# Performance work log

Hardware: AMD Instinct MI355X
Metric: run time of the kernel (lower is better)

Reference implementation:

```python
import jax, jax.numpy as jnp
import numpy as np

D_MODEL = 256; N_LAYERS = 4; INPUT_LEN = 15
D_INNER = 512; D_STATE = 16; D_CONV = 4; DT_RANK = 16
BATCH = 4; SEQ = 2048; EPS = 1e-5

def _ln(x, w, b):
    m = jnp.mean(x, -1, keepdims=True)
    v = jnp.var(x, -1, keepdims=True)
    return (x - m) * jax.lax.rsqrt(v + EPS) * w + b

def _silu(x):
    return x * jax.nn.sigmoid(x)

def _mixer(h, inW, cw, cb, xpW, dtW, dtb, A_log, Dp, opW):
    # h: [B,L,d_model]
    xz = h @ inW.T                      # [B,L,2*D_INNER]
    xh, z = jnp.split(xz, 2, axis=-1)
    # causal depthwise conv1d
    xc = jnp.transpose(xh, (0, 2, 1))   # [B,D,L]
    xc = jax.lax.conv_general_dilated(xc, cw, (1,), [(D_CONV - 1, 0)],
                                      feature_group_count=D_INNER,
                                      dimension_numbers=('NCH', 'OIH', 'NCH'))
    xc = xc + cb[None, :, None]
    xh = _silu(jnp.transpose(xc, (0, 2, 1)))  # [B,L,D]
    dbl = xh @ xpW.T                    # [B,L,DT_RANK+2N]
    dt = dbl[..., :DT_RANK]
    Bm = dbl[..., DT_RANK:DT_RANK + D_STATE]
    C = dbl[..., DT_RANK + D_STATE:]
    dt = jax.nn.softplus(dt @ dtW.T + dtb)    # [B,L,D]
    A = -jnp.exp(A_log)                       # [D,N]
    dA = jnp.exp(dt[..., None] * A)           # [B,L,D,N]
    dBu = dt[..., None] * Bm[:, :, None, :] * xh[..., None]  # [B,L,D,N]
    def step(hst, inp):
        dA_t, dBu_t, C_t = inp
        hst = dA_t * hst + dBu_t
        y = jnp.einsum('bdn,bn->bd', hst, C_t)
        return hst, y
    h0 = jnp.zeros((xh.shape[0], D_INNER, D_STATE), xh.dtype)
    _, ys = jax.lax.scan(step, h0, (jnp.transpose(dA, (1, 0, 2, 3)),
                                    jnp.transpose(dBu, (1, 0, 2, 3)),
                                    jnp.transpose(C, (1, 0, 2))))
    y = jnp.transpose(ys, (1, 0, 2)) + Dp * xh
    y = y * _silu(z)
    return y @ opW.T

def setup_inputs():
    key = jax.random.key(0)
    ks = jax.random.split(key, 8)
    s = 0.02
    return {
        'x_src': jax.random.normal(ks[0], (BATCH, SEQ, INPUT_LEN), jnp.float32),
        'single_eval_pos': 1024,
        'in_W': jax.random.normal(ks[1], (D_MODEL, INPUT_LEN)) * s,
        'norm_w': jnp.ones((N_LAYERS, D_MODEL)),
        'norm_b': jnp.zeros((N_LAYERS, D_MODEL)),
        'inproj_W': jax.random.normal(ks[2], (N_LAYERS, 2 * D_INNER, D_MODEL)) * s,
        'conv_w': jax.random.normal(ks[3], (N_LAYERS, D_INNER, 1, D_CONV)) * 0.2,
        'conv_b': jnp.zeros((N_LAYERS, D_INNER)),
        'xproj_W': jax.random.normal(ks[4], (N_LAYERS, DT_RANK + 2 * D_STATE, D_INNER)) * s,
        'dtproj_W': jax.random.normal(ks[5], (N_LAYERS, D_INNER, DT_RANK)) * 0.1,
        'dtproj_b': jnp.log(jnp.expm1(jnp.full((N_LAYERS, D_INNER), 0.01))),
        'A_log': jnp.log(jnp.broadcast_to(jnp.arange(1, D_STATE + 1, dtype=jnp.float32), (N_LAYERS, D_INNER, D_STATE)) + 0.0),
        'D_param': jnp.ones((N_LAYERS, D_INNER)),
        'outproj_W': jax.random.normal(ks[6], (N_LAYERS, D_MODEL, D_INNER)) * s,
        'out_W': jax.random.normal(ks[7], (1, D_MODEL)) * s,
    }

def reference(x_src, single_eval_pos, in_W, norm_w, norm_b, inproj_W, conv_w, conv_b, xproj_W, dtproj_W, dtproj_b, A_log, D_param, outproj_W, out_W):
    h = x_src @ in_W.T                  # [B,L,d_model]
    res = None
    for i in range(N_LAYERS):
        res = h if res is None else h + res
        hn = _ln(res, norm_w[i], norm_b[i])
        h = _mixer(hn, inproj_W[i], conv_w[i], conv_b[i], xproj_W[i],
                   dtproj_W[i], dtproj_b[i], A_log[i], D_param[i], outproj_W[i])
    # backbone returns hidden_states directly (norm_f defined but not applied)
    return h @ out_W.T                  # [B,L,1]
```

## Files before the change

kernel.cpp:

```cpp
#include <hip/hip_runtime.h>

#define B_   4
#define T_   2048
#define BT_  8192
#define INL  15
#define DM   256
#define DI   512
#define DX   1024
#define DS_  16
#define DR_  16
#define NO_  48
#define NL   4
#define NC_  128
#define LCH  16

#define N0C  (NL*DX*DM/4)
#define N1C  (NL*DM*DI/4)
#define N2C  (NL*NO_*DI/4)
#define NCVT ((N0C + N1C + N2C + DI + 255)/256)
#define NINL (BT_/4)

typedef short bf16x8 __attribute__((ext_vector_type(8)));
typedef float f32x4  __attribute__((ext_vector_type(4)));

__device__ __forceinline__ float sigmoidf_(float x){
    return __builtin_amdgcn_rcpf(1.f + __expf(-x));
}
__device__ __forceinline__ float softplusf_(float x){
    return fmaxf(x, 0.f) + __logf(1.f + __expf(-fabsf(x)));
}

__device__ __forceinline__ unsigned short f2bf(float x){
    union { float f; unsigned u; } v; v.f = x;
    unsigned r = (v.u + 0x7FFFu + ((v.u >> 16) & 1u)) >> 16;
    return (unsigned short)r;
}
__device__ __forceinline__ float bf2f(unsigned short h){
    union { unsigned u; float f; } v; v.u = ((unsigned)h) << 16;
    return v.f;
}

__device__ __forceinline__ void ld16(const float* __restrict__ p, float* v){
    const float4* q = (const float4*)p;
    float4 x0=q[0],x1=q[1],x2=q[2],x3=q[3];
    v[0]=x0.x; v[1]=x0.y; v[2]=x0.z; v[3]=x0.w;
    v[4]=x1.x; v[5]=x1.y; v[6]=x1.z; v[7]=x1.w;
    v[8]=x2.x; v[9]=x2.y; v[10]=x2.z; v[11]=x2.w;
    v[12]=x3.x; v[13]=x3.y; v[14]=x3.z; v[15]=x3.w;
}
__device__ __forceinline__ void st16(float* __restrict__ p, const float* v){
    float4* q = (float4*)p;
    q[0] = make_float4(v[0],v[1],v[2],v[3]);
    q[1] = make_float4(v[4],v[5],v[6],v[7]);
    q[2] = make_float4(v[8],v[9],v[10],v[11]);
    q[3] = make_float4(v[12],v[13],v[14],v[15]);
}

__global__ void k_init(const float* __restrict__ W0, unsigned short* __restrict__ h0,
                       unsigned short* __restrict__ l0,
                       const float* __restrict__ W1, unsigned short* __restrict__ h1,
                       unsigned short* __restrict__ l1,
                       const float* __restrict__ W2, unsigned short* __restrict__ h2,
                       unsigned short* __restrict__ l2,
                       const float* __restrict__ opW3, const float* __restrict__ outW,
                       float* __restrict__ cwc,
                       const float* __restrict__ x, const float* __restrict__ W,
                       float* __restrict__ res,
                       unsigned short* __restrict__ hnhi, unsigned short* __restrict__ hnlo,
                       const float* __restrict__ w, const float* __restrict__ b){
    int bid = blockIdx.x;
    if(bid < NCVT){
        int g = bid*256 + threadIdx.x;
        const float* Wp; unsigned short *hi, *lo; int idx;
        if(g < N0C){ Wp = W0; hi = h0; lo = l0; idx = g; }
        else if(g < N0C+N1C){ Wp = W1; hi = h1; lo = l1; idx = g - N0C; }
        else if(g < N0C+N1C+N2C){ Wp = W2; hi = h2; lo = l2; idx = g - N0C - N1C; }
        else {
            int k = g - (N0C+N1C+N2C);
            if(k < DI){
                float s = 0.f;
#pragma unroll 8
                for(int m=0;m<DM;m++) s += outW[m]*opW3[(size_t)m*DI + k];
                cwc[k] = s;
            }
            return;
        }
        float4 v = ((const float4*)Wp)[idx];
        ushort4 h, l;
        h.x = f2bf(v.x); l.x = f2bf(v.x - bf2f(h.x));
        h.y = f2bf(v.y); l.y = f2bf(v.y - bf2f(h.y));
        h.z = f2bf(v.z); l.z = f2bf(v.z - bf2f(h.z));
        h.w = f2bf(v.w); l.w = f2bf(v.w - bf2f(h.w));
        ((ushort4*)hi)[idx] = h;
        ((ushort4*)lo)[idx] = l;
        return;
    }
    int wv = threadIdx.x >> 6, lane = threadIdx.x & 63;
    int bt = (bid - NCVT)*4 + wv;
    const float* xr = x + bt*INL;
    float xl[INL];
#pragma unroll
    for(int k=0;k<INL;k++) xl[k] = xr[k];
    float4 v;
    float* vv = (float*)&v;
#pragma unroll
    for(int j=0;j<4;j++){
        int m = lane*4 + j;
        const float* wr = W + m*INL;
        float acc = 0.f;
#pragma unroll
        for(int k=0;k<INL;k++) acc += xl[k]*wr[k];
        vv[j] = acc;
    }
    ((float4*)(res + (size_t)bt*DM))[lane] = v;
    float s  = v.x+v.y+v.z+v.w;
    float ss = v.x*v.x+v.y*v.y+v.z*v.z+v.w*v.w;
#pragma unroll
    for(int m=1;m<64;m<<=1){ s += __shfl_xor(s,m); ss += __shfl_xor(ss,m); }
    float mean = s*(1.f/DM);
    float var  = ss*(1.f/DM) - mean*mean;
    float inv  = rsqrtf(var + 1e-5f);
    float4 wt = ((const float4*)w)[lane];
    float4 bs = ((const float4*)b)[lane];
    float4 o;
    o.x = (v.x-mean)*inv*wt.x + bs.x;
    o.y = (v.y-mean)*inv*wt.y + bs.y;
    o.z = (v.z-mean)*inv*wt.z + bs.z;
    o.w = (v.w-mean)*inv*wt.w + bs.w;
    ushort4 hh, ll;
    hh.x = f2bf(o.x); ll.x = f2bf(o.x - bf2f(hh.x));
    hh.y = f2bf(o.y); ll.y = f2bf(o.y - bf2f(hh.y));
    hh.z = f2bf(o.z); ll.z = f2bf(o.z - bf2f(hh.z));
    hh.w = f2bf(o.w); ll.w = f2bf(o.w - bf2f(hh.w));
    ((ushort4*)(hnhi + (size_t)bt*DM))[lane] = hh;
    ((ushort4*)(hnlo + (size_t)bt*DM))[lane] = ll;
}

__global__ void k_resln(const float* __restrict__ res,
                        unsigned short* __restrict__ hnhi, unsigned short* __restrict__ hnlo,
                        const float* __restrict__ w, const float* __restrict__ b){
    int wv = threadIdx.x >> 6, lane = threadIdx.x & 63;
    int bt = blockIdx.x*4 + wv;
    float4 v = ((const float4*)(res + (size_t)bt*DM))[lane];
    float s  = v.x+v.y+v.z+v.w;
    float ss = v.x*v.x+v.y*v.y+v.z*v.z+v.w*v.w;
#pragma unroll
    for(int m=1;m<64;m<<=1){ s += __shfl_xor(s,m); ss += __shfl_xor(ss,m); }
    float mean = s*(1.f/DM);
    float var  = ss*(1.f/DM) - mean*mean;
    float inv  = rsqrtf(var + 1e-5f);
    float4 wt = ((const float4*)w)[lane];
    float4 bs = ((const float4*)b)[lane];
    float4 o;
    o.x = (v.x-mean)*inv*wt.x + bs.x;
    o.y = (v.y-mean)*inv*wt.y + bs.y;
    o.z = (v.z-mean)*inv*wt.z + bs.z;
    o.w = (v.w-mean)*inv*wt.w + bs.w;
    ushort4 hh, ll;
    hh.x = f2bf(o.x); ll.x = f2bf(o.x - bf2f(hh.x));
    hh.y = f2bf(o.y); ll.y = f2bf(o.y - bf2f(hh.y));
    hh.z = f2bf(o.z); ll.z = f2bf(o.z - bf2f(hh.z));
    hh.w = f2bf(o.w); ll.w = f2bf(o.w - bf2f(hh.w));
    ((ushort4*)(hnhi + (size_t)bt*DM))[lane] = hh;
    ((ushort4*)(hnlo + (size_t)bt*DM))[lane] = ll;
}

template<int BM,int BN>
__global__ void __launch_bounds__(256) k_gemm_bf3(
    const unsigned short* __restrict__ Ahi, const unsigned short* __restrict__ Alo,
    const unsigned short* __restrict__ Bhi, const unsigned short* __restrict__ Blo,
    float* __restrict__ C, int M, int N, int K)
{
    constexpr int LDP = 40;
    constexpr int WM = BM/2, WN = BN/2;
    constexpr int MI_ = WM/16, NI_ = WN/16;
    __shared__ unsigned short sAh[BM*LDP], sAl[BM*LDP], sBh[BN*LDP], sBl[BN*LDP];
    int tid  = threadIdx.x;
    int wave = tid >> 6, lane = tid & 63;
    int wm0  = (wave >> 1) * WM, wn0 = (wave & 1) * WN;
    int m0   = blockIdx.y * BM, n0 = blockIdx.x * BN;
    int lr   = lane & 15;
    int kq   = (lane >> 4) * 8;
    int quad4 = (lane >> 4) * 4;

    f32x4 acc[MI_][NI_];
#pragma unroll
    for(int i=0;i<MI_;i++)
#pragma unroll
        for(int j=0;j<NI_;j++) acc[i][j] = (f32x4){0.f,0.f,0.f,0.f};

    for(int k0=0;k0<K;k0+=32){
#pragma unroll
        for(int i=tid;i<BM*4;i+=256){
            int r = i>>2, cg2 = (i&3)*8;
            size_t go = (size_t)(m0+r)*K + k0 + cg2;
            *(float4*)(&sAh[r*LDP + cg2]) = *(const float4*)(Ahi + go);
            *(float4*)(&sAl[r*LDP + cg2]) = *(const float4*)(Alo + go);
        }
#pragma unroll
        for(int i=tid;i<BN*4;i+=256){
            int r = i>>2, cg2 = (i&3)*8;
            size_t go = (size_t)(n0+r)*K + k0 + cg2;
            *(float4*)(&sBh[r*LDP + cg2]) = *(const float4*)(Bhi + go);
            *(float4*)(&sBl[r*LDP + cg2]) = *(const float4*)(Blo + go);
        }
        __syncthreads();
        bf16x8 ah[MI_], al[MI_], bh[NI_], bl[NI_];
#pragma unroll
        for(int mi=0;mi<MI_;mi++){
            int ro = (wm0 + mi*16 + lr)*LDP + kq;
            ah[mi] = *(const bf16x8*)(&sAh[ro]);
            al[mi] = *(const bf16x8*)(&sAl[ro]);
        }
#pragma unroll
        for(int ni=0;ni<NI_;ni++){
            int ro = (wn0 + ni*16 + lr)*LDP + kq;
            bh[ni] = *(const bf16x8*)(&sBh[ro]);
            bl[ni] = *(const bf16x8*)(&sBl[ro]);
        }
#pragma unroll
        for(int mi=0;mi<MI_;mi++)
#pragma unroll
            for(int ni=0;ni<NI_;ni++){
                acc[mi][ni] = __builtin_amdgcn_mfma_f32_16x16x32_bf16(ah[mi], bh[ni], acc[mi][ni], 0,0,0);
                acc[mi][ni] = __builtin_amdgcn_mfma_f32_16x16x32_bf16(ah[mi], bl[ni], acc[mi][ni], 0,0,0);
                acc[mi][ni] = __builtin_amdgcn_mfma_f32_16x16x32_bf16(al[mi], bh[ni], acc[mi][ni], 0,0,0);
            }
        __syncthreads();
    }
#pragma unroll
    for(int mi=0;mi<MI_;mi++)
#pragma unroll
        for(int ni=0;ni<NI_;ni++){
            int col = n0 + wn0 + ni*16 + lr;
#pragma unroll
            for(int r=0;r<4;r++){
                int row = m0 + wm0 + mi*16 + quad4 + r;
                C[(size_t)row*N + col] = acc[mi][ni][r];
            }
        }
}

__global__ void __launch_bounds__(256) k_gemm_pk_res(
    const unsigned* __restrict__ Apk,
    const unsigned short* __restrict__ Bhi, const unsigned short* __restrict__ Blo,
    float* __restrict__ res)
{
    constexpr int BM = 64, BN = 64, K = 512, LDP = 40;
    __shared__ unsigned short sAh[BM*LDP], sAl[BM*LDP], sBh[BN*LDP], sBl[BN*LDP];
    int tid  = threadIdx.x;
    int wave = tid >> 6, lane = tid & 63;
    int wm0  = (wave >> 1) * 32, wn0 = (wave & 1) * 32;
    int m0   = blockIdx.y * BM, n0 = blockIdx.x * BN;
    int lr   = lane & 15;
    int kq   = (lane >> 4) * 8;
    int quad4 = (lane >> 4) * 4;

    f32x4 acc[2][2];
#pragma unroll
    for(int i=0;i<2;i++)
#pragma unroll
        for(int j=0;j<2;j++) acc[i][j] = (f32x4){0.f,0.f,0.f,0.f};

    for(int k0=0;k0<K;k0+=32){
        if(tid < BM*2){
            int r = tid>>1, hf = (tid&1)*16;
            const uint4* yp = (const uint4*)(Apk + (size_t)(m0+r)*K + k0 + hf);
#pragma unroll
            for(int q=0;q<4;q++){
                uint4 p = yp[q];
                ushort4 H, L;
                H.x=(unsigned short)p.x;  L.x=(unsigned short)(p.x>>16);
                H.y=(unsigned short)p.y;  L.y=(unsigned short)(p.y>>16);
                H.z=(unsigned short)p.z;  L.z=(unsigned short)(p.z>>16);
                H.w=(unsigned short)p.w;  L.w=(unsigned short)(p.w>>16);
                *(ushort4*)(&sAh[r*LDP + hf + q*4]) = H;
                *(ushort4*)(&sAl[r*LDP + hf + q*4]) = L;
            }
        }
        {
            int r = tid>>2, cg2 = (tid&3)*8;
            size_t go = (size_t)(n0+r)*K + k0 + cg2;
            *(float4*)(&sBh[r*LDP + cg2]) = *(const float4*)(Bhi + go);
            *(float4*)(&sBl[r*LDP + cg2]) = *(const float4*)(Blo + go);
        }
        __syncthreads();
        bf16x8 ah[2], al[2], bh[2], bl[2];
#pragma unroll
        for(int mi=0;mi<2;mi++){
            int ro = (wm0 + mi*16 + lr)*LDP + kq;
            ah[mi] = *(const bf16x8*)(&sAh[ro]);
            al[mi] = *(const bf16x8*)(&sAl[ro]);
        }
#pragma unroll
        for(int ni=0;ni<2;ni++){
            int ro = (wn0 + ni*16 + lr)*LDP + kq;
            bh[ni] = *(const bf16x8*)(&sBh[ro]);
            bl[ni] = *(const bf16x8*)(&sBl[ro]);
        }
#pragma unroll
        for(int mi=0;mi<2;mi++)
#pragma unroll
            for(int ni=0;ni<2;ni++){
                acc[mi][ni] = __builtin_amdgcn_mfma_f32_16x16x32_bf16(ah[mi], bh[ni], acc[mi][ni], 0,0,0);
                acc[mi][ni] = __builtin_amdgcn_mfma_f32_16x16x32_bf16(ah[mi], bl[ni], acc[mi][ni], 0,0,0);
                acc[mi][ni] = __builtin_amdgcn_mfma_f32_16x16x32_bf16(al[mi], bh[ni], acc[mi][ni], 0,0,0);
            }
        __syncthreads();
    }
#pragma unroll
    for(int mi=0;mi<2;mi++)
#pragma unroll
        for(int ni=0;ni<2;ni++){
            int col = n0 + wn0 + ni*16 + lr;
#pragma unroll
            for(int r=0;r<4;r++){
                int row = m0 + wm0 + mi*16 + quad4 + r;
                size_t o = (size_t)row*DM + col;
                res[o] += acc[mi][ni][r];
            }
        }
}

__global__ void __launch_bounds__(512) k_convxp2(
    const float* __restrict__ xz, const float* __restrict__ cw, const float* __restrict__ cb,
    const unsigned short* __restrict__ Bhi, const unsigned short* __restrict__ Blo,
    const float* __restrict__ dtW, const float* __restrict__ dtbias,
    const float* __restrict__ A_log,
    float* __restrict__ dbl,
    float* __restrict__ S, float* __restrict__ sdt)
{
    __shared__ unsigned short sAh[16*520], sAl[16*520];
    __shared__ float sP[6][16][20];
    __shared__ float sD[16*52];

    int tid = threadIdx.x;
    int wave = tid >> 6, lane = tid & 63;
    int lr = lane & 15, kq = (lane>>4)*8, quad4 = (lane>>4)*4;
    int m0 = blockIdx.x * LCH;
    int d  = tid;
    int nt = wave >> 1, kh = wave & 1;

    float xv[19];
    {
        int rbase = m0 - 3;
        bool mask0 = ((m0 & (T_-1)) == 0);
#pragma unroll
        for(int j=0;j<19;j++)
            xv[j] = (mask0 && j<3) ? 0.f : xz[(size_t)(rbase+j)*DX + d];
    }
    float4 w4 = *(const float4*)(cw + d*4);
    float bias = cb[d];
    float vh[16];
#pragma unroll
    for(int t=0;t<16;t++){
        float a = bias + w4.x*xv[t] + w4.y*xv[t+1] + w4.z*xv[t+2] + w4.w*xv[t+3];
        float v = a * sigmoidf_(a);
        vh[t] = v;
        unsigned short hh = f2bf(v);
        sAh[t*520 + d] = hh;
        sAl[t*520 + d] = f2bf(v - bf2f(hh));
    }
    __syncthreads();

    if(wave < 6){
        const unsigned short* bhp = Bhi + (size_t)(nt*16 + lr)*DI + kh*256 + kq;
        const unsigned short* blp = Blo + (size_t)(nt*16 + lr)*DI + kh*256 + kq;
        f32x4 acc = {0.f,0.f,0.f,0.f};
#pragma unroll 4
        for(int ks=0;ks<8;ks++){
            int ao = lr*520 + kh*256 + ks*32 + kq;
            bf16x8 ah = *(const bf16x8*)(&sAh[ao]);
            bf16x8 al = *(const bf16x8*)(&sAl[ao]);
            bf16x8 bh = *(const bf16x8*)(bhp + ks*32);
            bf16x8 bl = *(const bf16x8*)(blp + ks*32);
            acc = __builtin_amdgcn_mfma_f32_16x16x32_bf16(ah, bh, acc, 0,0,0);
            acc = __builtin_amdgcn_mfma_f32_16x16x32_bf16(ah, bl, acc, 0,0,0);
            acc = __builtin_amdgcn_mfma_f32_16x16x32_bf16(al, bh, acc, 0,0,0);
        }
#pragma unroll
        for(int r=0;r<4;r++) sP[wave][quad4+r][lr] = acc[r];
    }
    __syncthreads();

    for(int i=tid;i<768;i+=512){
        int t = i/48, n = i - t*48;
        int nt2 = n >> 4, nn = n & 15;
        float v = sP[nt2*2][t][nn] + sP[nt2*2+1][t][nn];
        dbl[(size_t)(m0+t)*48 + n] = v;
        sD[t*52 + n] = v;
    }
    __syncthreads();

    float a_[16]; ld16(A_log + (size_t)d*16, a_);
#pragma unroll
    for(int n=0;n<16;n++) a_[n] = -__expf(a_[n]);
    float wr_[16]; ld16(dtW + (size_t)d*16, wr_);
    float bsv = dtbias[d];
    int b = m0 >> 11;
    int c = (m0 & (T_-1)) >> 4;
    float st_[16];
#pragma unroll
    for(int n=0;n<16;n++) st_[n] = 0.f;
    float sd = 0.f;
#pragma unroll 4
    for(int t=0;t<16;t++){
        float dl[16]; ld16(&sD[t*52], dl);
        float bv[16]; ld16(&sD[t*52 + 16], bv);
        float pre = bsv;
#pragma unroll
        for(int r=0;r<16;r++) pre += dl[r]*wr_[r];
        float dtv = softplusf_(pre);
        float dx = dtv*vh[t];
        sd += dtv;
#pragma unroll
        for(int n=0;n<16;n++) st_[n] = __expf(dtv*a_[n])*st_[n] + dx*bv[n];
    }
    st16(S + (((size_t)b*NC_ + c)*DI + d)*16, st_);
    sdt[((size_t)b*NC_ + c)*DI + d] = sd;
}

__global__ void k_scan2(const float* __restrict__ S, const float* __restrict__ sdt,
                        const float* __restrict__ A_log, float* __restrict__ Hinit){
    int g = blockIdx.x*128 + threadIdx.x;
    int b = g >> 13;
    int dn = g & 8191;
    int d = dn >> 4;
    float a = -__expf(A_log[dn]);
    float H = 0.f;
    for(int c0=0;c0<NC_;c0+=8){
        float sv[8], gv[8];
#pragma unroll
        for(int j=0;j<8;j++){
            sv[j] = S[((size_t)(b*NC_ + c0 + j))*8192 + dn];
            gv[j] = sdt[(size_t)(b*NC_ + c0 + j)*DI + d];
        }
#pragma unroll
        for(int j=0;j<8;j++){
            size_t o = ((size_t)(b*NC_ + c0 + j))*8192 + dn;
            Hinit[o] = H;
            H = __expf(gv[j]*a)*H + sv[j];
        }
    }
}

__global__ void __launch_bounds__(256) k_scan3(
    const float* __restrict__ dbl, const float* __restrict__ xz,
    const float* __restrict__ cvw, const float* __restrict__ cvb,
    const float* __restrict__ A_log, const float* __restrict__ Dpar,
    const float* __restrict__ dtW, const float* __restrict__ dtbias,
    const float* __restrict__ Hinit, unsigned* __restrict__ Y)
{
    __shared__ float sbc[16*52];
    int tid = threadIdx.x;
    int c = blockIdx.y, b = blockIdx.z;
    int m0 = b*T_ + c*LCH;
    if(tid < 192){
        int t = tid/12, s = tid - t*12;
        *(float4*)(&sbc[t*52 + s*4]) = *(const float4*)(dbl + (size_t)(m0+t)*48 + s*4);
    }
    __syncthreads();
    int d = blockIdx.x*256 + tid;
    float xv[19];
    {
        int rbase = m0 - 3;
        bool mask0 = (c == 0);
#pragma unroll
        for(int j=0;j<19;j++)
            xv[j] = (mask0 && j<3) ? 0.f : xz[(size_t)(rbase+j)*DX + d];
    }
    float zvp[16];
#pragma unroll
    for(int t=0;t<16;t++) zvp[t] = xz[(size_t)(m0+t)*DX + DI + d];
    float4 w4 = *(const float4*)(cvw + d*4);
    float bias = cvb[d];
    float xhp[16];
#pragma unroll
    for(int t=0;t<16;t++){
        float a = bias + w4.x*xv[t] + w4.y*xv[t+1] + w4.z*xv[t+2] + w4.w*xv[t+3];
        xhp[t] = a * sigmoidf_(a);
    }
    float a_[16]; ld16(A_log + (size_t)d*16, a_);
#pragma unroll
    for(int n=0;n<16;n++) a_[n] = -__expf(a_[n]);
    float wr_[16]; ld16(dtW + (size_t)d*16, wr_);
    float bsv = dtbias[d];
    float st_[16]; ld16(Hinit + (((size_t)b*NC_ + c)*DI + d)*16, st_);
    float Dp = Dpar[d];
#pragma unroll 2
    for(int t=0;t<LCH;t++){
        int bt = m0 + t;
        float dl[16]; ld16(&sbc[t*52], dl);
        float bv[16]; ld16(&sbc[t*52 + 16], bv);
        float cv[16]; ld16(&sbc[t*52 + 32], cv);
        float pre = bsv;
#pragma unroll
        for(int r=0;r<16;r++) pre += dl[r]*wr_[r];
        float dtv = softplusf_(pre);
        float xhv = xhp[t];
        float dx = dtv*xhv;
        float y = 0.f;
#pragma unroll
        for(int n=0;n<16;n++){
            st_[n] = __expf(dtv*a_[n])*st_[n] + dx*bv[n];
            y += st_[n]*cv[n];
        }
        float zv = zvp[t];
        y += Dp*xhv;
        y = y * zv * sigmoidf_(zv);
        unsigned short hh = f2bf(y);
        unsigned short ll = f2bf(y - bf2f(hh));
        Y[(size_t)bt*DI + d] = (unsigned)hh | ((unsigned)ll << 16);
    }
}

__global__ void __launch_bounds__(512) k_scan3o(
    const float* __restrict__ dbl, const float* __restrict__ xz,
    const float* __restrict__ cvw, const float* __restrict__ cvb,
    const float* __restrict__ A_log, const float* __restrict__ Dpar,
    const float* __restrict__ dtW, const float* __restrict__ dtbias,
    const float* __restrict__ Hinit, const float* __restrict__ cwc,
    float* __restrict__ out)
{
    __shared__ float sbc[16*52];
    __shared__ float sW[8][16];
    int tid = threadIdx.x;
    int c = blockIdx.x, b = blockIdx.y;
    int m0 = b*T_ + c*LCH;
    if(tid < 192){
        int t = tid/12, s = tid - t*12;
        *(float4*)(&sbc[t*52 + s*4]) = *(const float4*)(dbl + (size_t)(m0+t)*48 + s*4);
    }
    __syncthreads();
    int d = tid;
    int wave = tid >> 6, lane = tid & 63;
    float xv[19];
    {
        int rbase = m0 - 3;
        bool mask0 = (c == 0);
#pragma unroll
        for(int j=0;j<19;j++)
            xv[j] = (mask0 && j<3) ? 0.f : xz[(size_t)(rbase+j)*DX + d];
    }
    float zvp[16];
#pragma unroll
    for(int t=0;t<16;t++) zvp[t] = xz[(size_t)(m0+t)*DX + DI + d];
    float4 w4 = *(const float4*)(cvw + d*4);
    float bias = cvb[d];
    float xhp[16];
#pragma unroll
    for(int t=0;t<16;t++){
        float a = bias + w4.x*xv[t] + w4.y*xv[t+1] + w4.z*xv[t+2] + w4.w*xv[t+3];
        xhp[t] = a * sigmoidf_(a);
    }
    float a_[16]; ld16(A_log + (size_t)d*16, a_);
#pragma unroll
    for(int n=0;n<16;n++) a_[n] = -__expf(a_[n]);
    float wr_[16]; ld16(dtW + (size_t)d*16, wr_);
    float bsv = dtbias[d];
    float st_[16]; ld16(Hinit + (((size_t)b*NC_ + c)*DI + d)*16, st_);
    float Dp = Dpar[d];
    float cwv = cwc[d];
#pragma unroll 2
    for(int t=0;t<LCH;t++){
        float dl[16]; ld16(&sbc[t*52], dl);
        float bv[16]; ld16(&sbc[t*52 + 16], bv);
        float cv[16]; ld16(&sbc[t*52 + 32], cv);
        float pre = bsv;
#pragma unroll
        for(int r=0;r<16;r++) pre += dl[r]*wr_[r];
        float dtv = softplusf_(pre);
        float xhv = xhp[t];
        float dx = dtv*xhv;
        float y = 0.f;
#pragma unroll
        for(int n=0;n<16;n++){
            st_[n] = __expf(dtv*a_[n])*st_[n] + dx*bv[n];
            y += st_[n]*cv[n];
        }
        float zv = zvp[t];
        y += Dp*xhv;
        y = y * zv * sigmoidf_(zv);
        float s = y * cwv;
#pragma unroll
        for(int m=1;m<64;m<<=1) s += __shfl_xor(s,m);
        if(lane==0) sW[wave][t] = s;
    }
    __syncthreads();
    if(tid < 16){
        float s = 0.f;
#pragma unroll
        for(int w=0;w<8;w++) s += sW[w][tid];
        out[m0 + tid] = s;
    }
}

extern "C" void kernel_launch(void* const* d_in, const int* in_sizes, int n_in,
                              void* d_out, int out_size, void* d_ws, size_t ws_size,
                              hipStream_t stream){
    const float* x_src    = (const float*)d_in[0];
    const float* in_W     = (const float*)d_in[2];
    const float* norm_w   = (const float*)d_in[3];
    const float* norm_b   = (const float*)d_in[4];
    const float* inproj_W = (const float*)d_in[5];
    const float* conv_w   = (const float*)d_in[6];
    const float* conv_b   = (const float*)d_in[7];
    const float* xproj_W  = (const float*)d_in[8];
    const float* dtproj_W = (const float*)d_in[9];
    const float* dtproj_b = (const float*)d_in[10];
    const float* A_log    = (const float*)d_in[11];
    const float* D_param  = (const float*)d_in[12];
    const float* outproj_W= (const float*)d_in[13];
    const float* out_W    = (const float*)d_in[14];

    float* ws  = (float*)d_ws;
    float* res  = ws;
    float* xz   = res  + (size_t)BT_*DM;
    float* dbl  = xz   + (size_t)BT_*DX;
    float* sdtb = dbl  + (size_t)BT_*48;
    float* Sbuf = sdtb + (size_t)B_*NC_*DI;
    float* Hbuf = Sbuf + (size_t)B_*NC_*DI*DS_;
    unsigned short* us = (unsigned short*)(Hbuf + (size_t)B_*NC_*DI*DS_);
    unsigned short* WhiIn  = us;
    unsigned short* WloIn  = WhiIn  + (size_t)NL*DX*DM;
    unsigned short* WhiOut = WloIn  + (size_t)NL*DX*DM;
    unsigned short* WloOut = WhiOut + (size_t)NL*DM*DI;
    unsigned short* WhiXp  = WloOut + (size_t)NL*DM*DI;
    unsigned short* WloXp  = WhiXp  + (size_t)NL*NO_*DI;
    unsigned short* hnhi   = WloXp  + (size_t)NL*NO_*DI;
    unsigned short* hnlo   = hnhi   + (size_t)BT_*DM;
    unsigned*       ybuf   = (unsigned*)(hnlo + (size_t)BT_*DM);
    float*          cwb    = (float*)(ybuf + (size_t)BT_*DI);

    k_init<<<NCVT + NINL, 256, 0, stream>>>(
        inproj_W,  WhiIn,  WloIn,
        outproj_W, WhiOut, WloOut,
        xproj_W,   WhiXp,  WloXp,
        outproj_W + (size_t)3*DM*DI, out_W, cwb,
        x_src, in_W, res, hnhi, hnlo, norm_w, norm_b);
    for(int i=0;i<NL;i++){
        k_gemm_bf3<64,128><<<dim3(DX/128, BT_/64), 256, 0, stream>>>(
            hnhi, hnlo, WhiIn + (size_t)i*DX*DM, WloIn + (size_t)i*DX*DM, xz, BT_, DX, DM);
        k_convxp2<<<BT_/LCH, 512, 0, stream>>>(xz, conv_w + i*DI*4, conv_b + i*DI,
            WhiXp + (size_t)i*NO_*DI, WloXp + (size_t)i*NO_*DI,
            dtproj_W + (size_t)i*DI*DR_, dtproj_b + i*DI,
            A_log + (size_t)i*DI*DS_, dbl, Sbuf, sdtb);
        k_scan2<<<B_*DI*DS_/128, 128, 0, stream>>>(Sbuf, sdtb, A_log + (size_t)i*DI*DS_, Hbuf);
        if(i < NL-1){
            k_scan3<<<dim3(2, NC_, B_), 256, 0, stream>>>(dbl, xz,
                conv_w + i*DI*4, conv_b + i*DI,
                A_log + (size_t)i*DI*DS_, D_param + i*DI,
                dtproj_W + (size_t)i*DI*DR_, dtproj_b + i*DI, Hbuf, ybuf);
            k_gemm_pk_res<<<dim3(DM/64, BT_/64), 256, 0, stream>>>(
                ybuf, WhiOut + (size_t)i*DM*DI, WloOut + (size_t)i*DM*DI, res);
            k_resln<<<BT_/4, 256, 0, stream>>>(res, hnhi, hnlo,
                norm_w + (i+1)*DM, norm_b + (i+1)*DM);
        } else {
            k_scan3o<<<dim3(NC_, B_), 512, 0, stream>>>(dbl, xz,
                conv_w + i*DI*4, conv_b + i*DI,
                A_log + (size_t)i*DI*DS_, D_param + i*DI,
                dtproj_W + (size_t)i*DI*DR_, dtproj_b + i*DI, Hbuf, cwb,
                (float*)d_out);
        }
    }
}
```

Baseline: 529.6 us.

## Fuse conv/xproj, chunk scan, and output scan into one persistent kernel with grid barriers

Replaces the three per-layer kernels (conv+xproj+chunk-state, inter-chunk scan, intra-chunk output scan) with a single 512-block kernel that uses a software grid barrier between phases. The conv output, dt values and B/C projections stay in registers and LDS across phases, so the dbl buffer write and reload, the repeated conv and the softplus recomputation go away, along with two kernel launches per layer. The cost is that all 512 blocks must be co-resident for the spin barrier to be safe, which the launch bounds of 4 blocks per CU are meant to ensure. The inter-chunk scan phase also runs on only 64 threads per block while the rest wait.

```diff
diff --git a/kernel.cpp b/kernel.cpp
--- a/kernel.cpp
+++ b/kernel.cpp
@@ -13,6 +13,7 @@
 #define NL   4
 #define NC_  128
 #define LCH  16
+#define NBLK 512
 
 #define N0C  (NL*DX*DM/4)
 #define N1C  (NL*DM*DI/4)
@@ -54,6 +55,24 @@
     q[1] = make_float4(v[4],v[5],v[6],v[7]);
     q[2] = make_float4(v[8],v[9],v[10],v[11]);
     q[3] = make_float4(v[12],v[13],v[14],v[15]);
+}
+
+__device__ __forceinline__ void gbar(unsigned* cnt, unsigned* gen){
+    __syncthreads();
+    if(threadIdx.x == 0){
+        __threadfence();
+        unsigned g = __hip_atomic_load(gen, __ATOMIC_ACQUIRE, __HIP_MEMORY_SCOPE_AGENT);
+        unsigned a = __hip_atomic_fetch_add(cnt, 1u, __ATOMIC_ACQ_REL, __HIP_MEMORY_SCOPE_AGENT);
+        if(a == (unsigned)(NBLK-1)){
+            __hip_atomic_store(cnt, 0u, __ATOMIC_RELAXED, __HIP_MEMORY_SCOPE_AGENT);
+            __hip_atomic_store(gen, g+1u, __ATOMIC_RELEASE, __HIP_MEMORY_SCOPE_AGENT);
+        } else {
+            while(__hip_atomic_load(gen, __ATOMIC_ACQUIRE, __HIP_MEMORY_SCOPE_AGENT) == g)
+                __builtin_amdgcn_s_sleep(8);
+        }
+        __threadfence();
+    }
+    __syncthreads();
 }
 
 __global__ void k_init(const float* __restrict__ W0, unsigned short* __restrict__ h0,
@@ -67,8 +86,10 @@
                        const float* __restrict__ x, const float* __restrict__ W,
                        float* __restrict__ res,
                        unsigned short* __restrict__ hnhi, unsigned short* __restrict__ hnlo,
-                       const float* __restrict__ w, const float* __restrict__ b){
+                       const float* __restrict__ w, const float* __restrict__ b,
+                       unsigned* __restrict__ bcnt, unsigned* __restrict__ bgen){
     int bid = blockIdx.x;
+    if(bid == 0 && threadIdx.x == 0){ *bcnt = 0u; *bgen = 0u; }
     if(bid < NCVT){
         int g = bid*256 + threadIdx.x;
         const float* Wp; unsigned short *hi, *lo; int idx;
@@ -322,22 +343,25 @@
         }
 }
 
-__global__ void __launch_bounds__(512) k_convxp2(
-    const float* __restrict__ xz, const float* __restrict__ cw, const float* __restrict__ cb,
+__global__ void __launch_bounds__(512,4) k_scanall(
+    const float* __restrict__ xz, const float* __restrict__ cvw, const float* __restrict__ cvb,
     const unsigned short* __restrict__ Bhi, const unsigned short* __restrict__ Blo,
     const float* __restrict__ dtW, const float* __restrict__ dtbias,
-    const float* __restrict__ A_log,
-    float* __restrict__ dbl,
-    float* __restrict__ S, float* __restrict__ sdt)
+    const float* __restrict__ A_log, const float* __restrict__ Dpar,
+    float* __restrict__ S, float* __restrict__ sdt, float* __restrict__ Hinit,
+    unsigned* __restrict__ Y, const float* __restrict__ cwc, float* __restrict__ out,
+    unsigned* __restrict__ bcnt, unsigned* __restrict__ bgen, int last)
 {
     __shared__ unsigned short sAh[16*520], sAl[16*520];
     __shared__ float sP[6][16][20];
     __shared__ float sD[16*52];
+    __shared__ float sW[8][16];
 
     int tid = threadIdx.x;
     int wave = tid >> 6, lane = tid & 63;
     int lr = lane & 15, kq = (lane>>4)*8, quad4 = (lane>>4)*4;
-    int m0 = blockIdx.x * LCH;
+    int bid = blockIdx.x;
+    int m0 = bid * LCH;
     int d  = tid;
     int nt = wave >> 1, kh = wave & 1;
 
@@ -349,8 +373,8 @@
         for(int j=0;j<19;j++)
             xv[j] = (mask0 && j<3) ? 0.f : xz[(size_t)(rbase+j)*DX + d];
     }
-    float4 w4 = *(const float4*)(cw + d*4);
-    float bias = cb[d];
+    float4 w4 = *(const float4*)(cvw + d*4);
+    float bias = cvb[d];
     float vh[16];
 #pragma unroll
     for(int t=0;t<16;t++){
@@ -386,212 +410,122 @@
     for(int i=tid;i<768;i+=512){
         int t = i/48, n = i - t*48;
         int nt2 = n >> 4, nn = n & 15;
-        float v = sP[nt2*2][t][nn] + sP[nt2*2+1][t][nn];
-        dbl[(size_t)(m0+t)*48 + n] = v;
-        sD[t*52 + n] = v;
+        sD[t*52 + n] = sP[nt2*2][t][nn] + sP[nt2*2+1][t][nn];
     }
     __syncthreads();
 
     float a_[16]; ld16(A_log + (size_t)d*16, a_);
 #pragma unroll
     for(int n=0;n<16;n++) a_[n] = -__expf(a_[n]);
-    float wr_[16]; ld16(dtW + (size_t)d*16, wr_);
-    float bsv = dtbias[d];
     int b = m0 >> 11;
     int c = (m0 & (T_-1)) >> 4;
-    float st_[16];
-#pragma unroll
-    for(int n=0;n<16;n++) st_[n] = 0.f;
-    float sd = 0.f;
-#pragma unroll 4
-    for(int t=0;t<16;t++){
-        float dl[16]; ld16(&sD[t*52], dl);
-        float bv[16]; ld16(&sD[t*52 + 16], bv);
-        float pre = bsv;
-#pragma unroll
-        for(int r=0;r<16;r++) pre += dl[r]*wr_[r];
-        float dtv = softplusf_(pre);
-        float dx = dtv*vh[t];
-        sd += dtv;
-#pragma unroll
-        for(int n=0;n<16;n++) st_[n] = __expf(dtv*a_[n])*st_[n] + dx*bv[n];
-    }
-    st16(S + (((size_t)b*NC_ + c)*DI + d)*16, st_);
-    sdt[((size_t)b*NC_ + c)*DI + d] = sd;
-}
-
-__global__ void k_scan2(const float* __restrict__ S, const float* __restrict__ sdt,
-                        const float* __restrict__ A_log, float* __restrict__ Hinit){
-    int g = blockIdx.x*128 + threadIdx.x;
-    int b = g >> 13;
-    int dn = g & 8191;
-    int d = dn >> 4;
-    float a = -__expf(A_log[dn]);
-    float H = 0.f;
-    for(int c0=0;c0<NC_;c0+=8){
-        float sv[8], gv[8];
-#pragma unroll
-        for(int j=0;j<8;j++){
-            sv[j] = S[((size_t)(b*NC_ + c0 + j))*8192 + dn];
-            gv[j] = sdt[(size_t)(b*NC_ + c0 + j)*DI + d];
-        }
-#pragma unroll
-        for(int j=0;j<8;j++){
-            size_t o = ((size_t)(b*NC_ + c0 + j))*8192 + dn;
-            Hinit[o] = H;
-            H = __expf(gv[j]*a)*H + sv[j];
-        }
-    }
-}
-
-__global__ void __launch_bounds__(256) k_scan3(
-    const float* __restrict__ dbl, const float* __restrict__ xz,
-    const float* __restrict__ cvw, const float* __restrict__ cvb,
-    const float* __restrict__ A_log, const float* __restrict__ Dpar,
-    const float* __restrict__ dtW, const float* __restrict__ dtbias,
-    const float* __restrict__ Hinit, unsigned* __restrict__ Y)
-{
-    __shared__ float sbc[16*52];
-    int tid = threadIdx.x;
-    int c = blockIdx.y, b = blockIdx.z;
-    int m0 = b*T_ + c*LCH;
-    if(tid < 192){
-        int t = tid/12, s = tid - t*12;
-        *(float4*)(&sbc[t*52 + s*4]) = *(const float4*)(dbl + (size_t)(m0+t)*48 + s*4);
-    }
-    __syncthreads();
-    int d = blockIdx.x*256 + tid;
-    float xv[19];
+    float dtv_[16];
     {
-        int rbase = m0 - 3;
-        bool mask0 = (c == 0);
-#pragma unroll
-        for(int j=0;j<19;j++)
-            xv[j] = (mask0 && j<3) ? 0.f : xz[(size_t)(rbase+j)*DX + d];
-    }
+        float wr_[16]; ld16(dtW + (size_t)d*16, wr_);
+        float bsv = dtbias[d];
+        float st_[16];
+#pragma unroll
+        for(int n=0;n<16;n++) st_[n] = 0.f;
+        float sd = 0.f;
+#pragma unroll 2
+        for(int t=0;t<16;t++){
+            float dl[16]; ld16(&sD[t*52], dl);
+            float bv[16]; ld16(&sD[t*52 + 16], bv);
+            float pre = bsv;
+#pragma unroll
+            for(int r=0;r<16;r++) pre += dl[r]*wr_[r];
+            float dtv = softplusf_(pre);
+            dtv_[t] = dtv;
+            float dx = dtv*vh[t];
+            sd += dtv;
+#pragma unroll
+            for(int n=0;n<16;n++) st_[n] = __expf(dtv*a_[n])*st_[n] + dx*bv[n];
+        }
+        st16(S + (((size_t)b*NC_ + c)*DI + d)*16, st_);
+        sdt[((size_t)b*NC_ + c)*DI + d] = sd;
+    }
+
+    gbar(bcnt, bgen);
+
+    if(tid < 64){
+        int gid = bid*64 + tid;
+        int b2 = gid >> 13;
+        int dn = gid & 8191;
+        int d2 = dn >> 4;
+        float a = -__expf(A_log[dn]);
+        float H = 0.f;
+        for(int c0=0;c0<NC_;c0+=8){
+            float sv[8], gv[8];
+#pragma unroll
+            for(int j=0;j<8;j++){
+                sv[j] = S[((size_t)(b2*NC_ + c0 + j))*8192 + dn];
+                gv[j] = sdt[(size_t)(b2*NC_ + c0 + j)*DI + d2];
+            }
+#pragma unroll
+            for(int j=0;j<8;j++){
+                size_t o = ((size_t)(b2*NC_ + c0 + j))*8192 + dn;
+                Hinit[o] = H;
+                H = __expf(gv[j]*a)*H + sv[j];
+            }
+        }
+    }
+
+    gbar(bcnt, bgen);
+
     float zvp[16];
 #pragma unroll
     for(int t=0;t<16;t++) zvp[t] = xz[(size_t)(m0+t)*DX + DI + d];
-    float4 w4 = *(const float4*)(cvw + d*4);
-    float bias = cvb[d];
-    float xhp[16];
-#pragma unroll
-    for(int t=0;t<16;t++){
-        float a = bias + w4.x*xv[t] + w4.y*xv[t+1] + w4.z*xv[t+2] + w4.w*xv[t+3];
-        xhp[t] = a * sigmoidf_(a);
-    }
-    float a_[16]; ld16(A_log + (size_t)d*16, a_);
-#pragma unroll
-    for(int n=0;n<16;n++) a_[n] = -__expf(a_[n]);
-    float wr_[16]; ld16(dtW + (size_t)d*16, wr_);
-    float bsv = dtbias[d];
     float st_[16]; ld16(Hinit + (((size_t)b*NC_ + c)*DI + d)*16, st_);
     float Dp = Dpar[d];
+    if(!last){
 #pragma unroll 2
-    for(int t=0;t<LCH;t++){
-        int bt = m0 + t;
-        float dl[16]; ld16(&sbc[t*52], dl);
-        float bv[16]; ld16(&sbc[t*52 + 16], bv);
-        float cv[16]; ld16(&sbc[t*52 + 32], cv);
-        float pre = bsv;
-#pragma unroll
-        for(int r=0;r<16;r++) pre += dl[r]*wr_[r];
-        float dtv = softplusf_(pre);
-        float xhv = xhp[t];
-        float dx = dtv*xhv;
-        float y = 0.f;
-#pragma unroll
-        for(int n=0;n<16;n++){
-            st_[n] = __expf(dtv*a_[n])*st_[n] + dx*bv[n];
-            y += st_[n]*cv[n];
-        }
-        float zv = zvp[t];
-        y += Dp*xhv;
-        y = y * zv * sigmoidf_(zv);
-        unsigned short hh = f2bf(y);
-        unsigned short ll = f2bf(y - bf2f(hh));
-        Y[(size_t)bt*DI + d] = (unsigned)hh | ((unsigned)ll << 16);
-    }
-}
-
-__global__ void __launch_bounds__(512) k_scan3o(
-    const float* __restrict__ dbl, const float* __restrict__ xz,
-    const float* __restrict__ cvw, const float* __restrict__ cvb,
-    const float* __restrict__ A_log, const float* __restrict__ Dpar,
-    const float* __restrict__ dtW, const float* __restrict__ dtbias,
-    const float* __restrict__ Hinit, const float* __restrict__ cwc,
-    float* __restrict__ out)
-{
-    __shared__ float sbc[16*52];
-    __shared__ float sW[8][16];
-    int tid = threadIdx.x;
-    int c = blockIdx.x, b = blockIdx.y;
-    int m0 = b*T_ + c*LCH;
-    if(tid < 192){
-        int t = tid/12, s = tid - t*12;
-        *(float4*)(&sbc[t*52 + s*4]) = *(const float4*)(dbl + (size_t)(m0+t)*48 + s*4);
-    }
-    __syncthreads();
-    int d = tid;
-    int wave = tid >> 6, lane = tid & 63;
-    float xv[19];
-    {
-        int rbase = m0 - 3;
-        bool mask0 = (c == 0);
-#pragma unroll
-        for(int j=0;j<19;j++)
-            xv[j] = (mask0 && j<3) ? 0.f : xz[(size_t)(rbase+j)*DX + d];
-    }
-    float zvp[16];
-#pragma unroll
-    for(int t=0;t<16;t++) zvp[t] = xz[(size_t)(m0+t)*DX + DI + d];
-    float4 w4 = *(const float4*)(cvw + d*4);
-    float bias = cvb[d];
-    float xhp[16];
-#pragma unroll
-    for(int t=0;t<16;t++){
-        float a = bias + w4.x*xv[t] + w4.y*xv[t+1] + w4.z*xv[t+2] + w4.w*xv[t+3];
-        xhp[t] = a * sigmoidf_(a);
-    }
-    float a_[16]; ld16(A_log + (size_t)d*16, a_);
-#pragma unroll
-    for(int n=0;n<16;n++) a_[n] = -__expf(a_[n]);
-    float wr_[16]; ld16(dtW + (size_t)d*16, wr_);
-    float bsv = dtbias[d];
-    float st_[16]; ld16(Hinit + (((size_t)b*NC_ + c)*DI + d)*16, st_);
-    float Dp = Dpar[d];
-    float cwv = cwc[d];
+        for(int t=0;t<16;t++){
+            float bv[16]; ld16(&sD[t*52 + 16], bv);
+            float cv[16]; ld16(&sD[t*52 + 32], cv);
+            float dtv = dtv_[t];
+            float dx = dtv*vh[t];
+            float y = 0.f;
+#pragma unroll
+            for(int n=0;n<16;n++){
+                st_[n] = __expf(dtv*a_[n])*st_[n] + dx*bv[n];
+                y += st_[n]*cv[n];
+            }
+            float zv = zvp[t];
+            y += Dp*vh[t];
+            y = y * zv * sigmoidf_(zv);
+            unsigned short hh = f2bf(y);
+            unsigned short ll = f2bf(y - bf2f(hh));
+            Y[(size_t)(m0+t)*DI + d] = (unsigned)hh | ((unsigned)ll << 16);
+        }
+    } else {
+        float cwv = cwc[d];
 #pragma unroll 2
-    for(int t=0;t<LCH;t++){
-        float dl[16]; ld16(&sbc[t*52], dl);
-        float bv[16]; ld16(&sbc[t*52 + 16], bv);
-        float cv[16]; ld16(&sbc[t*52 + 32], cv);
-        float pre = bsv;
-#pragma unroll
-        for(int r=0;r<16;r++) pre += dl[r]*wr_[r];
-        float dtv = softplusf_(pre);
-        float xhv = xhp[t];
-        float dx = dtv*xhv;
-        float y = 0.f;
-#pragma unroll
-        for(int n=0;n<16;n++){
-            st_[n] = __expf(dtv*a_[n])*st_[n] + dx*bv[n];
-            y += st_[n]*cv[n];
-        }
-        float zv = zvp[t];
-        y += Dp*xhv;
-        y = y * zv * sigmoidf_(zv);
-        float s = y * cwv;
-#pragma unroll
-        for(int m=1;m<64;m<<=1) s += __shfl_xor(s,m);
-        if(lane==0) sW[wave][t] = s;
-    }
-    __syncthreads();
-    if(tid < 16){
-        float s = 0.f;
-#pragma unroll
-        for(int w=0;w<8;w++) s += sW[w][tid];
-        out[m0 + tid] = s;
+        for(int t=0;t<16;t++){
+            float bv[16]; ld16(&sD[t*52 + 16], bv);
+            float cv[16]; ld16(&sD[t*52 + 32], cv);
+            float dtv = dtv_[t];
+            float dx = dtv*vh[t];
+            float y = 0.f;
+#pragma unroll
+            for(int n=0;n<16;n++){
+                st_[n] = __expf(dtv*a_[n])*st_[n] + dx*bv[n];
+                y += st_[n]*cv[n];
+            }
+            float zv = zvp[t];
+            y += Dp*vh[t];
+            y = y * zv * sigmoidf_(zv);
+            float s = y * cwv;
+#pragma unroll
+            for(int m=1;m<64;m<<=1) s += __shfl_xor(s,m);
+            if(lane==0) sW[wave][t] = s;
+        }
+        __syncthreads();
+        if(tid < 16){
+            float s = 0.f;
+#pragma unroll
+            for(int w=0;w<8;w++) s += sW[w][tid];
+            out[m0 + tid] = s;
+        }
     }
 }
 
@@ -616,8 +550,7 @@
     float* ws  = (float*)d_ws;
     float* res  = ws;
     float* xz   = res  + (size_t)BT_*DM;
-    float* dbl  = xz   + (size_t)BT_*DX;
-    float* sdtb = dbl  + (size_t)BT_*48;
+    float* sdtb = xz   + (size_t)BT_*DX;
     float* Sbuf = sdtb + (size_t)B_*NC_*DI;
     float* Hbuf = Sbuf + (size_t)B_*NC_*DI*DS_;
     unsigned short* us = (unsigned short*)(Hbuf + (size_t)B_*NC_*DI*DS_);
@@ -631,36 +564,29 @@
     unsigned short* hnlo   = hnhi   + (size_t)BT_*DM;
     unsigned*       ybuf   = (unsigned*)(hnlo + (size_t)BT_*DM);
     float*          cwb    = (float*)(ybuf + (size_t)BT_*DI);
+    unsigned*       barv   = (unsigned*)(cwb + DI);
 
     k_init<<<NCVT + NINL, 256, 0, stream>>>(
         inproj_W,  WhiIn,  WloIn,
         outproj_W, WhiOut, WloOut,
         xproj_W,   WhiXp,  WloXp,
         outproj_W + (size_t)3*DM*DI, out_W, cwb,
-        x_src, in_W, res, hnhi, hnlo, norm_w, norm_b);
+        x_src, in_W, res, hnhi, hnlo, norm_w, norm_b,
+        barv, barv + 1);
     for(int i=0;i<NL;i++){
         k_gemm_bf3<64,128><<<dim3(DX/128, BT_/64), 256, 0, stream>>>(
             hnhi, hnlo, WhiIn + (size_t)i*DX*DM, WloIn + (size_t)i*DX*DM, xz, BT_, DX, DM);
-        k_convxp2<<<BT_/LCH, 512, 0, stream>>>(xz, conv_w + i*DI*4, conv_b + i*DI,
+        k_scanall<<<NBLK, 512, 0, stream>>>(xz, conv_w + i*DI*4, conv_b + i*DI,
             WhiXp + (size_t)i*NO_*DI, WloXp + (size_t)i*NO_*DI,
             dtproj_W + (size_t)i*DI*DR_, dtproj_b + i*DI,
-            A_log + (size_t)i*DI*DS_, dbl, Sbuf, sdtb);
-        k_scan2<<<B_*DI*DS_/128, 128, 0, stream>>>(Sbuf, sdtb, A_log + (size_t)i*DI*DS_, Hbuf);
+            A_log + (size_t)i*DI*DS_, D_param + i*DI,
+            Sbuf, sdtb, Hbuf, ybuf, cwb, (float*)d_out,
+            barv, barv + 1, (i == NL-1) ? 1 : 0);
         if(i < NL-1){
-            k_scan3<<<dim3(2, NC_, B_), 256, 0, stream>>>(dbl, xz,
-                conv_w + i*DI*4, conv_b + i*DI,
-                A_log + (size_t)i*DI*DS_, D_param + i*DI,
-                dtproj_W + (size_t)i*DI*DR_, dtproj_b + i*DI, Hbuf, ybuf);
             k_gemm_pk_res<<<dim3(DM/64, BT_/64), 256, 0, stream>>>(
                 ybuf, WhiOut + (size_t)i*DM*DI, WloOut + (size_t)i*DM*DI, res);
             k_resln<<<BT_/4, 256, 0, stream>>>(res, hnhi, hnlo,
                 norm_w + (i+1)*DM, norm_b + (i+1)*DM);
-        } else {
-            k_scan3o<<<dim3(NC_, B_), 512, 0, stream>>>(dbl, xz,
-                conv_w + i*DI*4, conv_b + i*DI,
-                A_log + (size_t)i*DI*DS_, D_param + i*DI,
-                dtproj_W + (size_t)i*DI*DR_, dtproj_b + i*DI, Hbuf, cwb,
-                (float*)d_out);
-        }
-    }
-}
+        }
+    }
+}
```

After: 1.205 ms. +127.5%, slower.
